# Kernel optimization log

Hardware: AMD Instinct MI355X
Metric: run time of the kernel (lower is better)

The kernel has to match this reference:

```python
import jax, jax.numpy as jnp
import numpy as np

D_MODEL = 1024
N_HEADS = 16
D_K = D_MODEL // N_HEADS
EPS = 1e-8


def _l2_rownorm(x):
    # RowNormActivation: normalize each row (last dim) to unit L2 norm
    return x * jax.lax.rsqrt(jnp.sum(x * x, axis=-1, keepdims=True) + EPS)


def setup_inputs() -> dict:
    key = jax.random.key(0)
    ks = jax.random.split(key, 11)
    B, S = 2, 2048
    sc = 1.0 / np.sqrt(D_MODEL)
    inp = {
        "Q": jax.random.normal(ks[0], (B, S, D_MODEL), jnp.float32),
        "K": jax.random.normal(ks[1], (B, S, D_MODEL), jnp.float32),
        "V": jax.random.normal(ks[2], (B, S, D_MODEL), jnp.float32),
        "Wq_w": jax.random.normal(ks[3], (D_MODEL, D_MODEL), jnp.float32) * sc,
        "Wq_b": jnp.zeros((D_MODEL,), jnp.float32),
        "Wk_w": jax.random.normal(ks[4], (D_MODEL, D_MODEL), jnp.float32) * sc,
        "Wk_b": jnp.zeros((D_MODEL,), jnp.float32),
        "Wv_w": jax.random.normal(ks[5], (D_MODEL, D_MODEL), jnp.float32) * sc,
        "Wv_b": jnp.zeros((D_MODEL,), jnp.float32),
        "Wo_w": jax.random.normal(ks[6], (D_MODEL, D_MODEL), jnp.float32) * sc,
        "Wo_b": jnp.zeros((D_MODEL,), jnp.float32),
    }
    return inp


def reference(Q, K, V, Wq_w, Wq_b, Wk_w, Wk_b, Wv_w, Wv_b, Wo_w, Wo_b):
    B, S, _ = Q.shape
    # torch Linear: y = x @ W.T + b
    q = (Q @ Wq_w.T + Wq_b).reshape(B, S, N_HEADS, D_K).transpose(0, 2, 1, 3)
    k = (K @ Wk_w.T + Wk_b).reshape(B, S, N_HEADS, D_K).transpose(0, 2, 1, 3)
    v = (V @ Wv_w.T + Wv_b).reshape(B, S, N_HEADS, D_K).transpose(0, 2, 1, 3)
    qn = _l2_rownorm(q)
    kn = _l2_rownorm(k)
    scores = jnp.einsum("bhqd,bhkd->bhqk", qn, kn)
    attn = scores * scores  # squared similarity, no softmax (dropout=0 / eval)
    out = jnp.einsum("bhqk,bhkd->bhqd", attn, v)
    out = out.transpose(0, 2, 1, 3).reshape(B, S, D_MODEL)
    return out @ Wo_w.T + Wo_b
```

## Files before the change

### kernel.cpp

```cpp
#include <hip/hip_runtime.h>
#include <hip/hip_bf16.h>


#define D_MODEL 1024
#define N_HEADS 16
#define D_K     64
#define BATCH   2
#define SEQ     2048
#define M_TOT   (BATCH * SEQ)

typedef short  s16x8 __attribute__((ext_vector_type(8)));
typedef short  s16x4 __attribute__((ext_vector_type(4)));
typedef float  f32x4 __attribute__((ext_vector_type(4)));
typedef unsigned short ushort_t;
typedef ushort_t us4 __attribute__((ext_vector_type(4)));
typedef ushort_t us8 __attribute__((ext_vector_type(8)));

__device__ __forceinline__ ushort_t f2bf(float f) {
    union { float f; unsigned int u; } x; x.f = f;
    unsigned int u = x.u;
    return (ushort_t)((u + 0x7fffu + ((u >> 16) & 1u)) >> 16);
}
__device__ __forceinline__ float bf2f(ushort_t h) {
    union { unsigned int u; float f; } x; x.u = ((unsigned int)h) << 16;
    return x.f;
}
__device__ __forceinline__ unsigned int pack2bf(float a, float b) {
    union { __hip_bfloat162 h; unsigned int u; } x;
    x.h = __float22bfloat162_rn(float2{a, b});
    return x.u;
}

__device__ __forceinline__ void gload_lds16(const ushort_t* g, ushort_t* l) {
    __builtin_amdgcn_global_load_lds(
        (__attribute__((address_space(1))) void*)(ushort_t*)g,
        (__attribute__((address_space(3))) void*)l, 16, 0, 0);
}

#define WAIT_VM(n)  asm volatile("s_waitcnt vmcnt(" #n ")" ::: "memory")
#define WAIT_LGKM0  asm volatile("s_waitcnt lgkmcnt(0)" ::: "memory")
#define BARRIER     asm volatile("s_barrier" ::: "memory")

struct ConvArgs {
    const float* src[11];
    ushort_t*    dst[11];
    int          n[11];
    int          cum[12];
};

__global__ __launch_bounds__(256) void convert_kernel(ConvArgs a) {
    const int lin = blockIdx.x;
    int t = 0;
#pragma unroll
    for (int i = 0; i < 11; ++i)
        if (lin >= a.cum[i + 1]) t = i + 1;
    const int off = (lin - a.cum[t]) * 2048 + threadIdx.x * 8;
    if (off >= a.n[t]) return;
    const float4 v0 = *(const float4*)(a.src[t] + off);
    const float4 v1 = *(const float4*)(a.src[t] + off + 4);
    us8 p;
    p[0] = f2bf(v0.x); p[1] = f2bf(v0.y); p[2] = f2bf(v0.z); p[3] = f2bf(v0.w);
    p[4] = f2bf(v1.x); p[5] = f2bf(v1.y); p[6] = f2bf(v1.z); p[7] = f2bf(v1.w);
    *(us8*)(a.dst[t] + off) = p;
}

template <int BM>
__device__ __forceinline__ void gemm_body(
    ushort_t* __restrict__ smem,
    const ushort_t* __restrict__ A,
    const ushort_t* __restrict__ W,
    const ushort_t* __restrict__ bias,
    float* __restrict__ outf,
    int bx, int by)
{
    static_assert(BM == 64 || BM == 128, "");
    constexpr int K    = 1024;
    constexpr int MF   = BM / 32;
    constexpr int BUFW = (BM + 128) * 64;
    constexpr int NIT  = K / 64;

    const int t    = threadIdx.x;
    const int wave = t >> 6;
    const int lane = t & 63;
    const int quad = lane >> 4;
    const int lc   = lane & 15;
    const int wm   = wave >> 1;
    const int wn   = wave & 1;
    const int m0   = bx * BM;
    const int n0   = by * 128;

    f32x4 acc[MF][4];
    const f32x4 zero = {0.f, 0.f, 0.f, 0.f};
#pragma unroll
    for (int i = 0; i < MF; ++i)
#pragma unroll
        for (int j = 0; j < 4; ++j) acc[i][j] = zero;

    auto stage = [&](int buf, int k0) {
        ushort_t* Ast = smem + buf * BUFW;
        ushort_t* Bst = Ast + BM * 64;
#pragma unroll
        for (int c = 0; c < MF; ++c) {
            int idx = c * 256 + t;
            int row = idx >> 3, phys = idx & 7;
            int col = (phys ^ (row & 7)) * 8;
            gload_lds16(A + (size_t)(m0 + row) * K + k0 + col, Ast + idx * 8);
        }
#pragma unroll
        for (int c = 0; c < 4; ++c) {
            int idx = c * 256 + t;
            int row = idx >> 3, phys = idx & 7;
            int col = (phys ^ (row & 7)) * 8;
            gload_lds16(W + (size_t)(n0 + row) * K + k0 + col, Bst + idx * 8);
        }
    };
    auto loadfrags = [&](int buf, s16x8 (&a)[MF][2], s16x8 (&b)[4][2]) {
        ushort_t* Ast = smem + buf * BUFW;
        ushort_t* Bst = Ast + BM * 64;
#pragma unroll
        for (int ks = 0; ks < 2; ++ks) {
            const int ph = ((ks * 4 + quad) ^ (lc & 7)) * 8;
#pragma unroll
            for (int i = 0; i < MF; ++i)
                a[i][ks] = *(const s16x8*)(Ast + (wm * (BM / 2) + i * 16 + lc) * 64 + ph);
#pragma unroll
            for (int i = 0; i < 4; ++i)
                b[i][ks] = *(const s16x8*)(Bst + (wn * 64 + i * 16 + lc) * 64 + ph);
        }
    };
    auto mfmas = [&](s16x8 (&a)[MF][2], s16x8 (&b)[4][2]) {
#pragma unroll
        for (int ks = 0; ks < 2; ++ks)
#pragma unroll
            for (int mf = 0; mf < MF; ++mf)
#pragma unroll
                for (int nf = 0; nf < 4; ++nf)
                    acc[mf][nf] = __builtin_amdgcn_mfma_f32_16x16x32_bf16(
                        a[mf][ks], b[nf][ks], acc[mf][nf], 0, 0, 0);
    };

    stage(0, 0);
    stage(1, 64);
    s16x8 afr[MF][2], bfr[4][2];
    for (int it = 0; it < NIT; ++it) {
        if (it < NIT - 1) {
            if constexpr (BM == 128) WAIT_VM(8); else WAIT_VM(6);
        } else {
            WAIT_VM(0);
        }
        BARRIER;
        loadfrags(it & 1, afr, bfr);
        WAIT_LGKM0;
        BARRIER;
        if (it < NIT - 2) stage(it & 1, (it + 2) * 64);
        mfmas(afr, bfr);
    }

    float bv[4];
#pragma unroll
    for (int nf = 0; nf < 4; ++nf) bv[nf] = bf2f(bias[n0 + wn * 64 + nf * 16 + lc]);

#pragma unroll
    for (int mf = 0; mf < MF; ++mf)
#pragma unroll
        for (int nf = 0; nf < 4; ++nf)
#pragma unroll
            for (int r = 0; r < 4; ++r) {
                int mg = m0 + wm * (BM / 2) + mf * 16 + quad * 4 + r;
                int ng = n0 + wn * 64 + nf * 16 + lc;
                outf[(size_t)mg * D_MODEL + ng] = acc[mf][nf][r] + bv[nf];
            }
}

template <int MODE>
__device__ __forceinline__ void gemm_body32(
    ushort_t* __restrict__ smem,
    const ushort_t* __restrict__ A,
    const ushort_t* __restrict__ W,
    const ushort_t* __restrict__ bias,
    ushort_t* __restrict__ out,
    int bx, int by)
{
    constexpr int K    = 1024;
    constexpr int BUFW = 256 * 32;
    constexpr int NIT  = K / 32;

    const int t    = threadIdx.x;
    const int wave = t >> 6;
    const int lane = t & 63;
    const int quad = lane >> 4;
    const int lc   = lane & 15;
    const int wm   = wave >> 1;
    const int wn   = wave & 1;
    const int m0   = bx * 128;
    const int n0   = by * 128;

    f32x4 acc[4][4];
    const f32x4 zero = {0.f, 0.f, 0.f, 0.f};
#pragma unroll
    for (int i = 0; i < 4; ++i)
#pragma unroll
        for (int j = 0; j < 4; ++j) acc[i][j] = zero;

    auto stage = [&](int buf, int k0) {
        ushort_t* Ast = smem + buf * BUFW;
        ushort_t* Bst = Ast + 128 * 32;
#pragma unroll
        for (int c = 0; c < 2; ++c) {
            int idx = c * 256 + t;
            int row = idx >> 2, phys = idx & 3;
            int col = (phys ^ (row & 3)) * 8;
            gload_lds16(A + (size_t)(m0 + row) * K + k0 + col, Ast + idx * 8);
        }
#pragma unroll
        for (int c = 0; c < 2; ++c) {
            int idx = c * 256 + t;
            int row = idx >> 2, phys = idx & 3;
            int col = (phys ^ (row & 3)) * 8;
            gload_lds16(W + (size_t)(n0 + row) * K + k0 + col, Bst + idx * 8);
        }
    };
    auto loadfrags = [&](int buf, s16x8 (&a)[4], s16x8 (&b)[4]) {
        ushort_t* Ast = smem + buf * BUFW;
        ushort_t* Bst = Ast + 128 * 32;
#pragma unroll
        for (int i = 0; i < 4; ++i) {
            int ra = wm * 64 + i * 16 + lc;
            a[i] = *(const s16x8*)(Ast + ra * 32 + ((quad ^ (ra & 3)) * 8));
            int rb = wn * 64 + i * 16 + lc;
            b[i] = *(const s16x8*)(Bst + rb * 32 + ((quad ^ (rb & 3)) * 8));
        }
    };
    auto mfmas = [&](s16x8 (&a)[4], s16x8 (&b)[4]) {
#pragma unroll
        for (int mf = 0; mf < 4; ++mf)
#pragma unroll
            for (int nf = 0; nf < 4; ++nf)
                acc[mf][nf] = __builtin_amdgcn_mfma_f32_16x16x32_bf16(
                    a[mf], b[nf], acc[mf][nf], 0, 0, 0);
    };

    stage(0, 0);
    stage(1, 32);
    s16x8 afr[4], bfr[4];
    for (int it = 0; it < NIT; ++it) {
        if (it < NIT - 1) { WAIT_VM(4); } else { WAIT_VM(0); }
        BARRIER;
        loadfrags(it & 1, afr, bfr);
        WAIT_LGKM0;
        BARRIER;
        if (it < NIT - 2) stage(it & 1, (it + 2) * 32);
        mfmas(afr, bfr);
    }

    float bv[4];
#pragma unroll
    for (int nf = 0; nf < 4; ++nf) bv[nf] = bf2f(bias[n0 + wn * 64 + nf * 16 + lc]);

    if (MODE == 1) {
#pragma unroll
        for (int mf = 0; mf < 4; ++mf)
#pragma unroll
            for (int r = 0; r < 4; ++r) {
                float ss = 0.f;
#pragma unroll
                for (int nf = 0; nf < 4; ++nf) {
                    float v = acc[mf][nf][r] + bv[nf];
                    acc[mf][nf][r] = v;
                    ss += v * v;
                }
                ss += __shfl_xor(ss, 1);
                ss += __shfl_xor(ss, 2);
                ss += __shfl_xor(ss, 4);
                ss += __shfl_xor(ss, 8);
                float inv = rsqrtf(ss + 1e-8f);
                int mg = m0 + wm * 64 + mf * 16 + quad * 4 + r;
                int b  = mg >> 11;
                int s  = mg & 2047;
#pragma unroll
                for (int nf = 0; nf < 4; ++nf) {
                    int ng = n0 + wn * 64 + nf * 16 + lc;
                    int h = ng >> 6, d = ng & 63;
                    out[(((size_t)(b * N_HEADS + h)) * SEQ + s) * D_K + d] =
                        f2bf(acc[mf][nf][r] * inv);
                }
            }
    } else {
        __syncthreads();
        ushort_t* vt = smem + wave * (64 * 72);
#pragma unroll
        for (int mf = 0; mf < 4; ++mf)
#pragma unroll
            for (int nf = 0; nf < 4; ++nf) {
                us4 p;
#pragma unroll
                for (int r = 0; r < 4; ++r) p[r] = f2bf(acc[mf][nf][r] + bv[nf]);
                *(us4*)(vt + (nf * 16 + lc) * 72 + mf * 16 + quad * 4) = p;
            }
        WAIT_LGKM0;
        __syncthreads();
#pragma unroll
        for (int r = 0; r < 8; ++r) {
            int d  = r * 8 + (lane >> 3);
            int so = (lane & 7) * 8;
            uint4 val = *(const uint4*)(vt + d * 72 + so);
            int mg = m0 + wm * 64 + so;
            int b  = mg >> 11;
            int s  = mg & 2047;
            int ng = n0 + wn * 64 + d;
            int h = ng >> 6, dh = ng & 63;
            *(uint4*)(out + (((size_t)(b * N_HEADS + h)) * D_K + dh) * SEQ + s) = val;
        }
    }
}

__global__ __launch_bounds__(256, 3) void qkv_kernel(
    const ushort_t* __restrict__ Qb, const ushort_t* __restrict__ Kb,
    const ushort_t* __restrict__ Vb,
    const ushort_t* __restrict__ Wq, const ushort_t* __restrict__ Wk,
    const ushort_t* __restrict__ Wv,
    const ushort_t* __restrict__ bq, const ushort_t* __restrict__ bk,
    const ushort_t* __restrict__ bv,
    ushort_t* __restrict__ qn, ushort_t* __restrict__ kn,
    ushort_t* __restrict__ vT)
{
    __shared__ __align__(16) ushort_t smem[18432];
    const int lin = blockIdx.x;
    const int by  = lin & 7;
    const int r   = lin >> 3;
    const int bx  = r & 31;
    const int z   = r >> 5;
    if (z == 0)
        gemm_body32<1>(smem, Qb, Wq, bq, qn, bx, by);
    else if (z == 1)
        gemm_body32<1>(smem, Kb, Wk, bk, kn, bx, by);
    else
        gemm_body32<2>(smem, Vb, Wv, bv, vT, bx, by);
}

__global__ __launch_bounds__(256) void wo_kernel(
    const ushort_t* __restrict__ A, const ushort_t* __restrict__ W,
    const ushort_t* __restrict__ bias, float* __restrict__ outf)
{
    __shared__ __align__(16) ushort_t smem[2 * (64 + 128) * 64];
    const int lin = blockIdx.x;
    gemm_body<64>(smem, A, W, bias, outf, lin >> 3, lin & 7);
}

__global__ __launch_bounds__(256, 2) void attn_kernel(
    const ushort_t* __restrict__ qn,
    const ushort_t* __restrict__ kn,
    const ushort_t* __restrict__ vT,
    ushort_t* __restrict__ attn_out)
{
    __shared__ __align__(16) ushort_t smem[4 * 8192];

    const int t    = threadIdx.x;
    const int wave = t >> 6;
    const int lane = t & 63;
    const int quad = lane >> 4;
    const int lc   = lane & 15;
    const int bh   = blockIdx.x;
    const int qt   = blockIdx.y;
    const int b    = bh >> 4;
    const int h    = bh & 15;

    const ushort_t* qb = qn + (size_t)bh * SEQ * D_K;
    const ushort_t* kb = kn + (size_t)bh * SEQ * D_K;
    const ushort_t* vb = vT + (size_t)bh * D_K * SEQ;
    const int q0 = qt * 128;

    s16x8 qf[8][2];
#pragma unroll
    for (int mf = 0; mf < 8; ++mf)
#pragma unroll
        for (int ks = 0; ks < 2; ++ks)
            qf[mf][ks] = *(const s16x8*)(qb + (size_t)(q0 + mf * 16 + lc) * D_K +
                                         ks * 32 + quad * 8);

    f32x4 oacc[4][8];
    const f32x4 zero = {0.f, 0.f, 0.f, 0.f};
#pragma unroll
    for (int df = 0; df < 4; ++df)
#pragma unroll
        for (int mf = 0; mf < 8; ++mf) oacc[df][mf] = zero;

    auto stage = [&](int buf, int j0) {
        ushort_t* kst = smem + buf * 8192;
        ushort_t* vst = kst + 4096;
#pragma unroll
        for (int c = 0; c < 2; ++c) {
            int idx = c * 256 + t;
            int row = idx >> 3, phys = idx & 7;
            int col = (phys ^ (row & 7)) * 8;
            gload_lds16(kb + (size_t)(j0 + row) * D_K + col, kst + idx * 8);
            gload_lds16(vb + (size_t)row * SEQ + j0 + col, vst + idx * 8);
        }
    };

    auto compute2 = [&](int ba, int bb) {
        ushort_t* kstA = smem + ba * 8192;
        ushort_t* vstA = kstA + 4096;
        ushort_t* kstB = smem + bb * 8192;
        ushort_t* vstB = kstB + 4096;
        s16x8 akA[2], akB[2];
#pragma unroll
        for (int ks = 0; ks < 2; ++ks) {
            const int off = (wave * 16 + lc) * 64 + (((ks * 4 + quad) ^ (lc & 7)) * 8);
            akA[ks] = *(const s16x8*)(kstA + off);
            akB[ks] = *(const s16x8*)(kstB + off);
        }
        s16x8 av[4];
#pragma unroll
        for (int df = 0; df < 4; ++df) {
            const int d  = df * 16 + lc;
            const int cj = wave * 2 + (quad >> 1);
            const int o  = d * 64 + ((cj ^ (d & 7)) << 3) + ((quad & 1) << 2);
            s16x4 lo = *(const s16x4*)(vstA + o);
            s16x4 hi = *(const s16x4*)(vstB + o);
            av[df] = s16x8{lo[0], lo[1], lo[2], lo[3], hi[0], hi[1], hi[2], hi[3]};
        }
#pragma unroll
        for (int mf = 0; mf < 8; ++mf) {
            f32x4 stA = zero, stB = zero;
#pragma unroll
            for (int ks = 0; ks < 2; ++ks) {
                stA = __builtin_amdgcn_mfma_f32_16x16x32_bf16(akA[ks], qf[mf][ks],
                                                              stA, 0, 0, 0);
                stB = __builtin_amdgcn_mfma_f32_16x16x32_bf16(akB[ks], qf[mf][ks],
                                                              stB, 0, 0, 0);
            }
            union { unsigned int u[4]; s16x8 v; } pb;
            pb.u[0] = pack2bf(stA[0] * stA[0], stA[1] * stA[1]);
            pb.u[1] = pack2bf(stA[2] * stA[2], stA[3] * stA[3]);
            pb.u[2] = pack2bf(stB[0] * stB[0], stB[1] * stB[1]);
            pb.u[3] = pack2bf(stB[2] * stB[2], stB[3] * stB[3]);
#pragma unroll
            for (int df = 0; df < 4; ++df)
                oacc[df][mf] = __builtin_amdgcn_mfma_f32_16x16x32_bf16(
                    av[df], pb.v, oacc[df][mf], 0, 0, 0);
        }
    };

    constexpr int NP = 16;
    stage(0, 0);
    stage(1, 64);
    stage(2, 128);
    stage(3, 192);
    for (int p = 0; p < NP; ++p) {
        if (p < NP - 1) { WAIT_VM(8); } else { WAIT_VM(0); }
        BARRIER;
        compute2((2 * p) & 3, (2 * p + 1) & 3);
        if (p < NP - 2) {
            WAIT_LGKM0;
            BARRIER;
            stage((2 * p) & 3, (2 * p + 4) * 64);
            stage((2 * p + 1) & 3, (2 * p + 5) * 64);
        }
    }

    float* red = (float*)smem;
    constexpr int RP = 17;
#pragma unroll
    for (int mf = 0; mf < 8; ++mf) {
        BARRIER;
#pragma unroll
        for (int df = 0; df < 4; ++df)
#pragma unroll
            for (int r = 0; r < 4; ++r)
                red[(wave * 64 + df * 16 + quad * 4 + r) * RP + lc] =
                    oacc[df][mf][r];
        WAIT_LGKM0;
        BARRIER;
#pragma unroll
        for (int qq = 0; qq < 4; ++qq) {
            const int q = wave * 4 + qq;
            const int d = lane;
            float v = red[(0 * 64 + d) * RP + q] + red[(1 * 64 + d) * RP + q] +
                      red[(2 * 64 + d) * RP + q] + red[(3 * 64 + d) * RP + q];
            const int s = q0 + mf * 16 + q;
            attn_out[((size_t)(b * SEQ + s)) * D_MODEL + h * D_K + d] = f2bf(v);
        }
    }
}

extern "C" void kernel_launch(void* const* d_in, const int* in_sizes, int n_in,
                              void* d_out, int out_size, void* d_ws, size_t ws_size,
                              hipStream_t stream)
{
    const float* Qf   = (const float*)d_in[0];
    const float* Kf   = (const float*)d_in[1];
    const float* Vf   = (const float*)d_in[2];
    const float* Wqf  = (const float*)d_in[3];
    const float* Wqbf = (const float*)d_in[4];
    const float* Wkf  = (const float*)d_in[5];
    const float* Wkbf = (const float*)d_in[6];
    const float* Wvf  = (const float*)d_in[7];
    const float* Wvbf = (const float*)d_in[8];
    const float* Wof  = (const float*)d_in[9];
    const float* Wobf = (const float*)d_in[10];

    const size_t NM = (size_t)M_TOT * D_MODEL;
    const size_t NW = (size_t)D_MODEL * D_MODEL;
    const size_t NB = D_MODEL;

    ushort_t* p = (ushort_t*)d_ws;
    ushort_t* Qb  = p;  p += NM;
    ushort_t* Kb  = p;  p += NM;
    ushort_t* Vb  = p;  p += NM;
    ushort_t* Wq  = p;  p += NW;
    ushort_t* Wk  = p;  p += NW;
    ushort_t* Wv  = p;  p += NW;
    ushort_t* Wo  = p;  p += NW;
    ushort_t* bq  = p;  p += NB;
    ushort_t* bk  = p;  p += NB;
    ushort_t* bvv = p;  p += NB;
    ushort_t* bo  = p;  p += NB;
    ushort_t* qn  = p;  p += NM;
    ushort_t* kn  = p;  p += NM;
    ushort_t* vT  = p;  p += NM;
    ushort_t* ao  = p;  p += NM;

    ConvArgs ca;
    ca.src[0] = Qf;   ca.dst[0] = Qb;  ca.n[0] = (int)NM;
    ca.src[1] = Kf;   ca.dst[1] = Kb;  ca.n[1] = (int)NM;
    ca.src[2] = Vf;   ca.dst[2] = Vb;  ca.n[2] = (int)NM;
    ca.src[3] = Wqf;  ca.dst[3] = Wq;  ca.n[3] = (int)NW;
    ca.src[4] = Wkf;  ca.dst[4] = Wk;  ca.n[4] = (int)NW;
    ca.src[5] = Wvf;  ca.dst[5] = Wv;  ca.n[5] = (int)NW;
    ca.src[6] = Wof;  ca.dst[6] = Wo;  ca.n[6] = (int)NW;
    ca.src[7] = Wqbf; ca.dst[7] = bq;  ca.n[7] = (int)NB;
    ca.src[8] = Wkbf; ca.dst[8] = bk;  ca.n[8] = (int)NB;
    ca.src[9] = Wvbf; ca.dst[9] = bvv; ca.n[9] = (int)NB;
    ca.src[10] = Wobf; ca.dst[10] = bo; ca.n[10] = (int)NB;

    int cum = 0;
    ca.cum[0] = 0;
    for (int i = 0; i < 11; ++i) {
        cum += (ca.n[i] + 2047) / 2048;
        ca.cum[i + 1] = cum;
    }

    dim3 blk(256);
    convert_kernel<<<dim3((unsigned)cum), blk, 0, stream>>>(ca);

    qkv_kernel<<<dim3(768), blk, 0, stream>>>(
        Qb, Kb, Vb, Wq, Wk, Wv, bq, bk, bvv, qn, kn, vT);
    attn_kernel<<<dim3(BATCH * N_HEADS, SEQ / 128), blk, 0, stream>>>(qn, kn, vT, ao);
    wo_kernel<<<dim3(512), blk, 0, stream>>>(
        ao, Wo, bo, (float*)d_out);
}
```

Baseline: 212.5 us.

## Fuse fp32-to-bf16 activation conversion into QKV GEMM loads

Activations Q/K/V are no longer converted to bf16 by a separate pass. The QKV GEMM instead loads fp32 tiles into registers, converts them and writes them to LDS, with a 3-deep W buffer and a 2-deep A buffer in a reworked pipeline. This removes a full read-write round trip over three large activation tensors. It also remaps block indices so each XCD works on a contiguous group of row tiles. The cost is more VGPR pressure, register-staged A loads instead of direct-to-LDS copies, and a larger LDS footprint per block.

```diff
diff --git a/kernel.cpp b/kernel.cpp
--- a/kernel.cpp
+++ b/kernel.cpp
@@ -42,17 +42,17 @@
 #define BARRIER     asm volatile("s_barrier" ::: "memory")
 
 struct ConvArgs {
-    const float* src[11];
-    ushort_t*    dst[11];
-    int          n[11];
-    int          cum[12];
+    const float* src[8];
+    ushort_t*    dst[8];
+    int          n[8];
+    int          cum[9];
 };
 
 __global__ __launch_bounds__(256) void convert_kernel(ConvArgs a) {
     const int lin = blockIdx.x;
     int t = 0;
 #pragma unroll
-    for (int i = 0; i < 11; ++i)
+    for (int i = 0; i < 8; ++i)
         if (lin >= a.cum[i + 1]) t = i + 1;
     const int off = (lin - a.cum[t]) * 2048 + threadIdx.x * 8;
     if (off >= a.n[t]) return;
@@ -173,17 +173,16 @@
 }
 
 template <int MODE>
-__device__ __forceinline__ void gemm_body32(
+__device__ __forceinline__ void gemm_body32f(
     ushort_t* __restrict__ smem,
-    const ushort_t* __restrict__ A,
+    const float* __restrict__ Af,
     const ushort_t* __restrict__ W,
     const ushort_t* __restrict__ bias,
     ushort_t* __restrict__ out,
     int bx, int by)
 {
-    constexpr int K    = 1024;
-    constexpr int BUFW = 256 * 32;
-    constexpr int NIT  = K / 32;
+    constexpr int K   = 1024;
+    constexpr int NIT = K / 32;
 
     const int t    = threadIdx.x;
     const int wave = t >> 6;
@@ -202,33 +201,50 @@
 #pragma unroll
         for (int j = 0; j < 4; ++j) acc[i][j] = zero;
 
-    auto stage = [&](int buf, int k0) {
-        ushort_t* Ast = smem + buf * BUFW;
-        ushort_t* Bst = Ast + 128 * 32;
+    float4 ar[4];
+    auto loadA = [&](int k0) {
 #pragma unroll
         for (int c = 0; c < 2; ++c) {
             int idx = c * 256 + t;
             int row = idx >> 2, phys = idx & 3;
             int col = (phys ^ (row & 3)) * 8;
-            gload_lds16(A + (size_t)(m0 + row) * K + k0 + col, Ast + idx * 8);
-        }
+            const float* src = Af + (size_t)(m0 + row) * K + k0 + col;
+            ar[c * 2]     = *(const float4*)(src);
+            ar[c * 2 + 1] = *(const float4*)(src + 4);
+        }
+    };
+    auto writeA = [&](int abuf) {
+        ushort_t* Ast = smem + abuf * 4096;
+#pragma unroll
+        for (int c = 0; c < 2; ++c) {
+            int idx = c * 256 + t;
+            us8 p;
+            p[0] = f2bf(ar[c * 2].x);     p[1] = f2bf(ar[c * 2].y);
+            p[2] = f2bf(ar[c * 2].z);     p[3] = f2bf(ar[c * 2].w);
+            p[4] = f2bf(ar[c * 2 + 1].x); p[5] = f2bf(ar[c * 2 + 1].y);
+            p[6] = f2bf(ar[c * 2 + 1].z); p[7] = f2bf(ar[c * 2 + 1].w);
+            *(us8*)(Ast + idx * 8) = p;
+        }
+    };
+    auto stageW = [&](int wbuf, int k0) {
+        ushort_t* Wst = smem + 8192 + wbuf * 4096;
 #pragma unroll
         for (int c = 0; c < 2; ++c) {
             int idx = c * 256 + t;
             int row = idx >> 2, phys = idx & 3;
             int col = (phys ^ (row & 3)) * 8;
-            gload_lds16(W + (size_t)(n0 + row) * K + k0 + col, Bst + idx * 8);
-        }
-    };
-    auto loadfrags = [&](int buf, s16x8 (&a)[4], s16x8 (&b)[4]) {
-        ushort_t* Ast = smem + buf * BUFW;
-        ushort_t* Bst = Ast + 128 * 32;
+            gload_lds16(W + (size_t)(n0 + row) * K + k0 + col, Wst + idx * 8);
+        }
+    };
+    auto loadfrags = [&](int abuf, int wbuf, s16x8 (&a)[4], s16x8 (&b)[4]) {
+        ushort_t* Ast = smem + abuf * 4096;
+        ushort_t* Wst = smem + 8192 + wbuf * 4096;
 #pragma unroll
         for (int i = 0; i < 4; ++i) {
             int ra = wm * 64 + i * 16 + lc;
             a[i] = *(const s16x8*)(Ast + ra * 32 + ((quad ^ (ra & 3)) * 8));
             int rb = wn * 64 + i * 16 + lc;
-            b[i] = *(const s16x8*)(Bst + rb * 32 + ((quad ^ (rb & 3)) * 8));
+            b[i] = *(const s16x8*)(Wst + rb * 32 + ((quad ^ (rb & 3)) * 8));
         }
     };
     auto mfmas = [&](s16x8 (&a)[4], s16x8 (&b)[4]) {
@@ -240,16 +256,29 @@
                     a[mf], b[nf], acc[mf][nf], 0, 0, 0);
     };
 
-    stage(0, 0);
-    stage(1, 32);
+    loadA(0);
+    stageW(0, 0);
+    stageW(1, 32);
+    WAIT_VM(4);
+    writeA(0);
+    loadA(32);
+    stageW(2, 64);
+    WAIT_VM(8);
+    WAIT_LGKM0;
+    BARRIER;
+
     s16x8 afr[4], bfr[4];
     for (int it = 0; it < NIT; ++it) {
-        if (it < NIT - 1) { WAIT_VM(4); } else { WAIT_VM(0); }
-        BARRIER;
-        loadfrags(it & 1, afr, bfr);
+        loadfrags(it & 1, it % 3, afr, bfr);
+        if (it < NIT - 1) {
+            if (it < NIT - 2) { WAIT_VM(2); }
+            else              { WAIT_VM(0); }
+            writeA((it + 1) & 1);
+        }
         WAIT_LGKM0;
         BARRIER;
-        if (it < NIT - 2) stage(it & 1, (it + 2) * 32);
+        if (it < NIT - 2) loadA((it + 2) * 32);
+        if (it < NIT - 3) stageW((it + 3) % 3, (it + 3) * 32);
         mfmas(afr, bfr);
     }
 
@@ -315,8 +344,8 @@
 }
 
 __global__ __launch_bounds__(256, 3) void qkv_kernel(
-    const ushort_t* __restrict__ Qb, const ushort_t* __restrict__ Kb,
-    const ushort_t* __restrict__ Vb,
+    const float* __restrict__ Qf, const float* __restrict__ Kf,
+    const float* __restrict__ Vf,
     const ushort_t* __restrict__ Wq, const ushort_t* __restrict__ Wk,
     const ushort_t* __restrict__ Wv,
     const ushort_t* __restrict__ bq, const ushort_t* __restrict__ bk,
@@ -324,18 +353,20 @@
     ushort_t* __restrict__ qn, ushort_t* __restrict__ kn,
     ushort_t* __restrict__ vT)
 {
-    __shared__ __align__(16) ushort_t smem[18432];
+    __shared__ __align__(16) ushort_t smem[20480];
     const int lin = blockIdx.x;
-    const int by  = lin & 7;
-    const int r   = lin >> 3;
-    const int bx  = r & 31;
-    const int z   = r >> 5;
+    const int xcd = lin & 7;
+    const int idx = lin >> 3;
+    const int zbx = xcd * 12 + (idx % 12);
+    const int by  = idx / 12;
+    const int z   = zbx >> 5;
+    const int bx  = zbx & 31;
     if (z == 0)
-        gemm_body32<1>(smem, Qb, Wq, bq, qn, bx, by);
+        gemm_body32f<1>(smem, Qf, Wq, bq, qn, bx, by);
     else if (z == 1)
-        gemm_body32<1>(smem, Kb, Wk, bk, kn, bx, by);
+        gemm_body32f<1>(smem, Kf, Wk, bk, kn, bx, by);
     else
-        gemm_body32<2>(smem, Vb, Wv, bv, vT, bx, by);
+        gemm_body32f<2>(smem, Vf, Wv, bv, vT, bx, by);
 }
 
 __global__ __launch_bounds__(256) void wo_kernel(
@@ -505,9 +536,6 @@
     const size_t NB = D_MODEL;
 
     ushort_t* p = (ushort_t*)d_ws;
-    ushort_t* Qb  = p;  p += NM;
-    ushort_t* Kb  = p;  p += NM;
-    ushort_t* Vb  = p;  p += NM;
     ushort_t* Wq  = p;  p += NW;
     ushort_t* Wk  = p;  p += NW;
     ushort_t* Wv  = p;  p += NW;
@@ -522,21 +550,18 @@
     ushort_t* ao  = p;  p += NM;
 
     ConvArgs ca;
-    ca.src[0] = Qf;   ca.dst[0] = Qb;  ca.n[0] = (int)NM;
-    ca.src[1] = Kf;   ca.dst[1] = Kb;  ca.n[1] = (int)NM;
-    ca.src[2] = Vf;   ca.dst[2] = Vb;  ca.n[2] = (int)NM;
-    ca.src[3] = Wqf;  ca.dst[3] = Wq;  ca.n[3] = (int)NW;
-    ca.src[4] = Wkf;  ca.dst[4] = Wk;  ca.n[4] = (int)NW;
-    ca.src[5] = Wvf;  ca.dst[5] = Wv;  ca.n[5] = (int)NW;
-    ca.src[6] = Wof;  ca.dst[6] = Wo;  ca.n[6] = (int)NW;
-    ca.src[7] = Wqbf; ca.dst[7] = bq;  ca.n[7] = (int)NB;
-    ca.src[8] = Wkbf; ca.dst[8] = bk;  ca.n[8] = (int)NB;
-    ca.src[9] = Wvbf; ca.dst[9] = bvv; ca.n[9] = (int)NB;
-    ca.src[10] = Wobf; ca.dst[10] = bo; ca.n[10] = (int)NB;
+    ca.src[0] = Wqf;  ca.dst[0] = Wq;  ca.n[0] = (int)NW;
+    ca.src[1] = Wkf;  ca.dst[1] = Wk;  ca.n[1] = (int)NW;
+    ca.src[2] = Wvf;  ca.dst[2] = Wv;  ca.n[2] = (int)NW;
+    ca.src[3] = Wof;  ca.dst[3] = Wo;  ca.n[3] = (int)NW;
+    ca.src[4] = Wqbf; ca.dst[4] = bq;  ca.n[4] = (int)NB;
+    ca.src[5] = Wkbf; ca.dst[5] = bk;  ca.n[5] = (int)NB;
+    ca.src[6] = Wvbf; ca.dst[6] = bvv; ca.n[6] = (int)NB;
+    ca.src[7] = Wobf; ca.dst[7] = bo;  ca.n[7] = (int)NB;
 
     int cum = 0;
     ca.cum[0] = 0;
-    for (int i = 0; i < 11; ++i) {
+    for (int i = 0; i < 8; ++i) {
         cum += (ca.n[i] + 2047) / 2048;
         ca.cum[i + 1] = cum;
     }
@@ -545,7 +570,7 @@
     convert_kernel<<<dim3((unsigned)cum), blk, 0, stream>>>(ca);
 
     qkv_kernel<<<dim3(768), blk, 0, stream>>>(
-        Qb, Kb, Vb, Wq, Wk, Wv, bq, bk, bvv, qn, kn, vT);
+        Qf, Kf, Vf, Wq, Wk, Wv, bq, bk, bvv, qn, kn, vT);
     attn_kernel<<<dim3(BATCH * N_HEADS, SEQ / 128), blk, 0, stream>>>(qn, kn, vT, ao);
     wo_kernel<<<dim3(512), blk, 0, stream>>>(
         ao, Wo, bo, (float*)d_out);
```

After: 211.2 us. No clear change (-0.6%).
